# Optimization experiments

Measured on AMD Instinct MI355X. Metric: run time of the kernel, lower is better.

The kernel has to match this reference:

```python
import jax, jax.numpy as jnp
import numpy as np

DIM = 1024
HEADS = 8


def setup_inputs() -> dict:
    key = jax.random.key(0)
    ks = jax.random.split(key, 8)
    b, n, m, nc, d = 2, 1024, 4, 1024, DIM
    x = jax.random.normal(ks[0], (b, n, d), dtype=jnp.float32)
    context = jax.random.normal(ks[1], (b, m, nc, d), dtype=jnp.float32)
    doc_similarities = jax.random.normal(ks[2], (b, m), dtype=jnp.float32)
    # learned params (Linear weights stored as [in, out] for x @ W)
    s = 1.0 / np.sqrt(d)
    Wq = jax.random.uniform(ks[3], (d, d), minval=-s, maxval=s, dtype=jnp.float32)
    Wkv = jax.random.uniform(ks[4], (d, 2 * d), minval=-s, maxval=s, dtype=jnp.float32)
    Wout = jax.random.uniform(ks[5], (d, d), minval=-s, maxval=s, dtype=jnp.float32)
    bout = jax.random.uniform(ks[6], (d,), minval=-s, maxval=s, dtype=jnp.float32)
    beta = jnp.array(1.0, dtype=jnp.float32)
    return {"x": x, "context": context, "doc_similarities": doc_similarities,
            "Wq": Wq, "Wkv": Wkv, "beta": beta, "Wout": Wout, "bout": bout}


def reference(x, context, doc_similarities, Wq, Wkv, beta, Wout, bout):
    b, n, dim = x.shape
    h = HEADS
    hd = dim // h
    scale = dim ** -0.5
    m, nc = context.shape[1], context.shape[2]

    # q: [b, h, n, hd]
    q = (x @ Wq).reshape(b, n, h, hd).transpose(0, 2, 1, 3)

    # flatten docs: [b, m*nc, dim]
    ctx = context.reshape(b, m * nc, dim)
    # doc similarity bias, repeated per token within each doc: [b, m*nc]
    sim = jnp.repeat(doc_similarities, nc, axis=1) * beta

    kv = ctx @ Wkv  # [b, L, 2*dim]
    k, v = jnp.split(kv, 2, axis=-1)
    k = k.reshape(b, m * nc, h, hd).transpose(0, 2, 1, 3)  # [b, h, L, hd]
    v = v.reshape(b, m * nc, h, hd).transpose(0, 2, 1, 3)

    dots = jnp.einsum('bhid,bhjd->bhij', q, k) * scale
    dots = dots + sim[:, None, None, :]
    attn = jax.nn.softmax(dots, axis=-1)
    out = jnp.einsum('bhij,bhjd->bhid', attn, v)
    out = out.transpose(0, 2, 1, 3).reshape(b, n, dim)
    return out @ Wout + bout
```

## Files before the change

### kernel.cpp

```cpp
#include <hip/hip_runtime.h>
#include <stdint.h>

typedef __attribute__((ext_vector_type(4))) float f32x4;
typedef __attribute__((ext_vector_type(8))) __bf16 bf16x8;

__device__ __forceinline__ uint16_t f2bf(float f) {
  uint32_t u = __builtin_bit_cast(uint32_t, f);
  u += 0x7FFFu + ((u >> 16) & 1u);
  return (uint16_t)(u >> 16);
}

__device__ __forceinline__ float bf2f(uint16_t u) {
  uint32_t v = ((uint32_t)u) << 16;
  return __builtin_bit_cast(float, v);
}

__device__ __forceinline__ void load_lds16(const uint16_t* g, uint16_t* l) {
  __builtin_amdgcn_global_load_lds((const __attribute__((address_space(1))) void*)g,
                                   (__attribute__((address_space(3))) void*)l, 16, 0, 0);
}

__global__ __launch_bounds__(256) void k_prep(const float* __restrict__ x,
                                              const float* __restrict__ ctx,
                                              const float* __restrict__ Wq,
                                              const float* __restrict__ Wkv,
                                              const float* __restrict__ Wout,
                                              uint16_t* __restrict__ xb,
                                              uint16_t* __restrict__ ctxb,
                                              uint16_t* __restrict__ wqt,
                                              uint16_t* __restrict__ wkvt,
                                              uint16_t* __restrict__ woutt,
                                              float qscale) {
  __shared__ float tile[32][33];
  int id = blockIdx.x;
  int tid = threadIdx.x;
  if (id < 10240) {
    const float* in;
    uint16_t* out;
    int j = id * 256 + tid;
    if (j < 524288) { in = x; out = xb; }
    else            { in = ctx; out = ctxb; j -= 524288; }
    float4 v = ((const float4*)in)[j];
    union { uint16_t u[4]; uint64_t q; } o;
    o.u[0] = f2bf(v.x); o.u[1] = f2bf(v.y); o.u[2] = f2bf(v.z); o.u[3] = f2bf(v.w);
    ((uint64_t*)out)[j] = o.q;
    return;
  }
  id -= 10240;
  const float* W;
  uint16_t* Wt;
  int N, n0, k0;
  float sc = 1.0f;
  if (id < 1024)      { W = Wq;   Wt = wqt;   N = 1024; sc = qscale;
                        n0 = (id & 31) * 32; k0 = (id >> 5) * 32; }
  else if (id < 2048) { W = Wout; Wt = woutt; N = 1024; id -= 1024;
                        n0 = (id & 31) * 32; k0 = (id >> 5) * 32; }
  else                { W = Wkv;  Wt = wkvt;  N = 2048; id -= 2048;
                        n0 = (id & 63) * 32; k0 = (id >> 6) * 32; }
  int c = tid & 31, r0 = tid >> 5;
#pragma unroll
  for (int i = 0; i < 4; i++) {
    int r = r0 + i * 8;
    tile[r][c] = W[(size_t)(k0 + r) * N + n0 + c];
  }
  __syncthreads();
#pragma unroll
  for (int i = 0; i < 4; i++) {
    int r = r0 + i * 8;
    Wt[(size_t)(n0 + r) * 1024 + k0 + c] = f2bf(tile[c][r] * sc);
  }
}

__global__ __launch_bounds__(256, 4) void k_gemm_fused(const uint16_t* __restrict__ ctxb,
                                                       const uint16_t* __restrict__ wkvt,
                                                       const uint16_t* __restrict__ xb,
                                                       const uint16_t* __restrict__ wqt,
                                                       uint16_t* __restrict__ kb,
                                                       uint16_t* __restrict__ vtb,
                                                       uint16_t* __restrict__ qb) {
  __shared__ uint16_t smem[16384];
  const int K = 1024;
  const int tid = threadIdx.x;
  const int lane = tid & 63, w = tid >> 6;
  const int quad = lane >> 4, l16 = lane & 15;
  const int wr = (w >> 1) * 64, wc = (w & 1) * 64;
  int id = blockIdx.x;
  int bx, by, isQ;
  const uint16_t *Ab, *Bb;
  if (id < 1024) {
    isQ = 0;
    int xcd = id & 7, t = id >> 3;
    by = (xcd << 3) + (t & 7);
    bx = t >> 3;
    Ab = ctxb + (size_t)by * 128 * K;
    Bb = wkvt + (size_t)bx * 128 * K;
  } else {
    isQ = 1; id -= 1024;
    int xcd = id & 7, t = id >> 3;
    by = (xcd << 1) + (t & 1);
    bx = t >> 1;
    Ab = xb + (size_t)by * 128 * K;
    Bb = wqt + (size_t)bx * 128 * K;
  }
  f32x4 acc[4][4] = {};
  const int rA = tid >> 2, slotA = tid & 3;
  const int rA1 = rA + 64;
  const int segA0 = (slotA ^ ((rA + (rA >> 2)) & 3)) * 8;
  const int segA1 = (slotA ^ ((rA1 + (rA1 >> 2)) & 3)) * 8;
  const uint16_t* gA0 = Ab + (size_t)rA * K + segA0;
  const uint16_t* gA1 = Ab + (size_t)rA1 * K + segA1;
  const uint16_t* gB0 = Bb + (size_t)rA * K + segA0;
  const uint16_t* gB1 = Bb + (size_t)rA1 * K + segA1;
  load_lds16(gA0, smem + tid * 8);
  load_lds16(gA1, smem + (tid + 256) * 8);
  load_lds16(gB0, smem + (tid + 512) * 8);
  load_lds16(gB1, smem + (tid + 768) * 8);
  for (int t = 0; t < 32; ++t) {
    const uint16_t* la = smem + (t & 1) * 8192;
    const uint16_t* lb = la + 4096;
    if (t < 31) {
      uint16_t* ln = smem + ((t + 1) & 1) * 8192;
      const int k1 = (t + 1) * 32;
      load_lds16(gA0 + k1, ln + tid * 8);
      load_lds16(gA1 + k1, ln + (tid + 256) * 8);
      load_lds16(gB0 + k1, ln + (tid + 512) * 8);
      load_lds16(gB1 + k1, ln + (tid + 768) * 8);
      asm volatile("s_waitcnt vmcnt(4)\n\ts_barrier" ::: "memory");
    } else {
      asm volatile("s_waitcnt vmcnt(0)\n\ts_barrier" ::: "memory");
    }
    bf16x8 af[4], bfr[4];
#pragma unroll
    for (int i = 0; i < 4; i++) {
      int R = wr + i * 16 + l16;
      int s = quad ^ ((R + (R >> 2)) & 3);
      af[i] = *(const bf16x8*)&la[R * 32 + s * 8];
    }
#pragma unroll
    for (int j = 0; j < 4; j++) {
      int R = wc + j * 16 + l16;
      int s = quad ^ ((R + (R >> 2)) & 3);
      bfr[j] = *(const bf16x8*)&lb[R * 32 + s * 8];
    }
    __builtin_amdgcn_s_setprio(1);
#pragma unroll
    for (int i = 0; i < 4; i++)
#pragma unroll
      for (int j = 0; j < 4; j++)
        acc[i][j] = __builtin_amdgcn_mfma_f32_16x16x32_bf16(af[i], bfr[j], acc[i][j], 0, 0, 0);
    __builtin_amdgcn_s_setprio(0);
    asm volatile("s_barrier" ::: "memory");
  }
  __syncthreads();
  if (isQ) {
#pragma unroll
    for (int i = 0; i < 4; i++)
#pragma unroll
      for (int j = 0; j < 4; j++) {
        size_t row = (size_t)by * 128 + wr + i * 16 + quad * 4;
        size_t col = (size_t)bx * 128 + wc + j * 16 + l16;
#pragma unroll
        for (int r = 0; r < 4; r++)
          qb[(row + r) * 1024 + col] = f2bf(acc[i][j][r]);
      }
  } else if (bx < 8) {
#pragma unroll
    for (int i = 0; i < 4; i++)
#pragma unroll
      for (int j = 0; j < 4; j++) {
        int rowg = by * 128 + wr + i * 16 + quad * 4;
        int bb = rowg >> 12, l = rowg & 4095;
        int c = wc + j * 16 + l16;
        uint16_t* dst = kb + (((size_t)(bb * 8 + bx) * 4096 + l) * 128 + c);
#pragma unroll
        for (int r = 0; r < 4; r++)
          dst[r * 128] = f2bf(acc[i][j][r]);
      }
  } else {
    const int bh = (by >> 5) * 8 + (bx - 8);
    const int lbase = (by & 31) * 128;
    uint16_t* vdst = vtb + (size_t)bh * 524288;
#pragma unroll
    for (int half = 0; half < 2; half++) {
      if (wr == half * 64) {
#pragma unroll
        for (int i = 0; i < 4; i++)
#pragma unroll
          for (int j = 0; j < 4; j++) {
            int rowl = i * 16 + quad * 4;
            int col = wc + j * 16 + l16;
            union { uint64_t q; uint16_t u[4]; } pk;
#pragma unroll
            for (int r = 0; r < 4; r++) pk.u[r] = f2bf(acc[i][j][r]);
            *(uint64_t*)&smem[col * 72 + rowl] = pk.q;
          }
      }
      __syncthreads();
      {
        int col = tid >> 1, rseg = (tid & 1) * 32;
        const uint16_t* src = &smem[col * 72 + rseg];
        uint16_t* d = vdst + (size_t)col * 4096 + lbase + half * 64 + rseg;
#pragma unroll
        for (int k = 0; k < 4; k++)
          ((uint4*)d)[k] = *(const uint4*)&src[k * 8];
      }
      __syncthreads();
    }
  }
}

__global__ __launch_bounds__(256) void k_gemm64(const uint16_t* __restrict__ A,
                                                const uint16_t* __restrict__ Bt,
                                                float* __restrict__ Cf,
                                                const float* __restrict__ bias,
                                                int M, int N, int K) {
  __shared__ uint16_t smem[16384];
  const int tid = threadIdx.x;
  const int lane = tid & 63, w = tid >> 6;
  const int quad = lane >> 4, l16 = lane & 15;
  const int wr = (w >> 1) * 32, wc = (w & 1) * 32;
  const size_t tr0 = (size_t)blockIdx.y * 64, tc0 = (size_t)blockIdx.x * 64;
  f32x4 acc[2][2] = {};
  const int rS = tid >> 3, sS = tid & 7;
  const int seg = (sS ^ (rS & 7)) * 8;
  const uint16_t* Ab = A + tr0 * K;
  const uint16_t* Bb = Bt + tc0 * K;
  const uint16_t* gA0 = Ab + (size_t)rS * K + seg;
  const uint16_t* gA1 = Ab + (size_t)(rS + 32) * K + seg;
  const uint16_t* gB0 = Bb + (size_t)rS * K + seg;
  const uint16_t* gB1 = Bb + (size_t)(rS + 32) * K + seg;
  const int NT = K >> 6;
  load_lds16(gA0, smem + tid * 8);
  load_lds16(gA1, smem + (tid + 256) * 8);
  load_lds16(gB0, smem + (tid + 512) * 8);
  load_lds16(gB1, smem + (tid + 768) * 8);
  for (int t = 0; t < NT; ++t) {
    const uint16_t* la = smem + (t & 1) * 8192;
    const uint16_t* lb = la + 4096;
    if (t < NT - 1) {
      uint16_t* ln = smem + ((t + 1) & 1) * 8192;
      const int k1 = (t + 1) * 64;
      load_lds16(gA0 + k1, ln + tid * 8);
      load_lds16(gA1 + k1, ln + (tid + 256) * 8);
      load_lds16(gB0 + k1, ln + (tid + 512) * 8);
      load_lds16(gB1 + k1, ln + (tid + 768) * 8);
      asm volatile("s_waitcnt vmcnt(4)\n\ts_barrier" ::: "memory");
    } else {
      asm volatile("s_waitcnt vmcnt(0)\n\ts_barrier" ::: "memory");
    }
    __builtin_amdgcn_s_setprio(1);
#pragma unroll
    for (int sub = 0; sub < 2; sub++) {
      const int kk = sub * 4 + quad;
      bf16x8 af[2], bfr[2];
#pragma unroll
      for (int i = 0; i < 2; i++) {
        int R = wr + i * 16 + l16;
        af[i] = *(const bf16x8*)&la[R * 64 + (kk ^ (R & 7)) * 8];
      }
#pragma unroll
      for (int j = 0; j < 2; j++) {
        int R = wc + j * 16 + l16;
        bfr[j] = *(const bf16x8*)&lb[R * 64 + (kk ^ (R & 7)) * 8];
      }
#pragma unroll
      for (int i = 0; i < 2; i++)
#pragma unroll
        for (int j = 0; j < 2; j++)
          acc[i][j] = __builtin_amdgcn_mfma_f32_16x16x32_bf16(af[i], bfr[j], acc[i][j], 0, 0, 0);
    }
    __builtin_amdgcn_s_setprio(0);
    asm volatile("s_barrier" ::: "memory");
  }
#pragma unroll
  for (int i = 0; i < 2; i++) {
#pragma unroll
    for (int j = 0; j < 2; j++) {
      size_t row = tr0 + wr + i * 16 + quad * 4;
      size_t col = tc0 + wc + j * 16 + l16;
#pragma unroll
      for (int r = 0; r < 4; r++)
        Cf[(row + r) * N + col] = acc[i][j][r] + bias[col];
    }
  }
}

__global__ __launch_bounds__(256) void k_attn(const uint16_t* __restrict__ q,
                                              const uint16_t* __restrict__ kb,
                                              const uint16_t* __restrict__ vt,
                                              const float* __restrict__ sims,
                                              const float* __restrict__ beta,
                                              uint16_t* __restrict__ po,
                                              float* __restrict__ pl) {
  __shared__ uint16_t Kl[2][8192];
  __shared__ uint16_t Vl[2][8192];
  __shared__ uint16_t Pl[4096];
  const int idx = blockIdx.x;
  const int qbx = idx >> 7, g = idx & 127;
  const int h = g >> 4, b = (g >> 3) & 1, sp = g & 7;
  const int q0 = qbx * 128;
  const int tid = threadIdx.x, lane = tid & 63, w = tid >> 6;
  const int quad = lane >> 4, l16 = lane & 15;
  const float wsplit =
      __builtin_amdgcn_exp2f(sims[b * 4 + (sp >> 1)] * beta[0] * 1.44269504f);
  uint16_t* Pw = Pl + w * 1024;

  union { uint32_t u[4]; bf16x8 v; } Oc;
#pragma unroll
  for (int j = 0; j < 4; j++) Oc.u[j] = 0x3F803F80u;
  const bf16x8 onesf = Oc.v;

  bf16x8 qf[2][4];
#pragma unroll
  for (int rb = 0; rb < 2; rb++) {
    const uint16_t* qrow =
        q + ((size_t)(b * 1024 + q0 + w * 32 + rb * 16 + l16)) * 1024 + h * 128 + quad * 8;
#pragma unroll
    for (int ks = 0; ks < 4; ks++) qf[rb][ks] = *(const bf16x8*)(qrow + ks * 32);
  }
  f32x4 o[2][8] = {};
  f32x4 o9[2] = {};

  const uint16_t* kptr = kb + ((size_t)(b * 8 + h) * 4096 + sp * 512) * 128;
  const uint16_t* vptr = vt + ((size_t)(b * 8 + h) * 128) * 4096 + sp * 512;

#pragma unroll
  for (int ii = 0; ii < 4; ii++) {
    int g2 = tid + ii * 256;
    int row = g2 >> 4, seg = (g2 & 15) ^ (row & 15);
    load_lds16(kptr + row * 128 + seg * 8, &Kl[0][g2 * 8]);
  }
#pragma unroll
  for (int ii = 0; ii < 4; ii++) {
    int g2 = tid + ii * 256;
    int row = g2 >> 3, seg = (g2 & 7) ^ (row & 7);
    load_lds16(vptr + (size_t)row * 4096 + seg * 8, &Vl[0][g2 * 8]);
  }

  for (int c = 0; c < 8; c++) {
    const uint16_t* Kc = Kl[c & 1];
    const uint16_t* Vc = Vl[c & 1];
    if (c < 7) {
      const uint16_t* kn = kptr + 64 * 128;
      const uint16_t* vn = vptr + 64;
      uint16_t* Kd = Kl[(c + 1) & 1];
      uint16_t* Vd = Vl[(c + 1) & 1];
#pragma unroll
      for (int ii = 0; ii < 4; ii++) {
        int g2 = tid + ii * 256;
        int row = g2 >> 4, seg = (g2 & 15) ^ (row & 15);
        load_lds16(kn + row * 128 + seg * 8, Kd + g2 * 8);
      }
#pragma unroll
      for (int ii = 0; ii < 4; ii++) {
        int g2 = tid + ii * 256;
        int row = g2 >> 3, seg = (g2 & 7) ^ (row & 7);
        load_lds16(vn + (size_t)row * 4096 + seg * 8, Vd + g2 * 8);
      }
      asm volatile("s_waitcnt vmcnt(8)\n\ts_barrier" ::: "memory");
    } else {
      asm volatile("s_waitcnt vmcnt(0)\n\ts_barrier" ::: "memory");
    }
#pragma unroll
    for (int kh = 0; kh < 2; kh++) {
#pragma unroll
      for (int nb2 = 0; nb2 < 2; nb2++) {
        const int nb = kh * 2 + nb2;
        f32x4 s0 = {}, s1 = {};
        __builtin_amdgcn_s_setprio(1);
#pragma unroll
        for (int ks = 0; ks < 4; ks++) {
          bf16x8 kf = *(const bf16x8*)&Kc[(nb * 16 + l16) * 128 + (((ks * 4 + quad) ^ l16) * 8)];
          s0 = __builtin_amdgcn_mfma_f32_16x16x32_bf16(qf[0][ks], kf, s0, 0, 0, 0);
          s1 = __builtin_amdgcn_mfma_f32_16x16x32_bf16(qf[1][ks], kf, s1, 0, 0, 0);
        }
        __builtin_amdgcn_s_setprio(0);
        const int sl = nb2 * 2 + (l16 >> 3);
#pragma unroll
        for (int r = 0; r < 4; r++) {
          int rp0 = quad * 4 + r;
          Pw[rp0 * 32 + ((sl ^ ((rp0 >> 1) & 3)) * 8) + (l16 & 7)] =
              f2bf(__builtin_amdgcn_exp2f(s0[r]));
          int rp1 = 16 + rp0;
          Pw[rp1 * 32 + ((sl ^ ((rp1 >> 1) & 3)) * 8) + (l16 & 7)] =
              f2bf(__builtin_amdgcn_exp2f(s1[r]));
        }
      }
      __asm__ volatile("s_waitcnt lgkmcnt(0)" ::: "memory");
      const int segp = (quad ^ ((l16 >> 1) & 3)) * 8;
      bf16x8 pf0 = *(const bf16x8*)&Pw[l16 * 32 + segp];
      bf16x8 pf1 = *(const bf16x8*)&Pw[(16 + l16) * 32 + segp];
      const int sq = ((kh * 4 + quad) ^ (l16 & 7)) * 8;
      __builtin_amdgcn_s_setprio(1);
#pragma unroll
      for (int nb = 0; nb < 8; nb++) {
        bf16x8 vf = *(const bf16x8*)&Vc[(nb * 16 + l16) * 64 + sq];
        o[0][nb] = __builtin_amdgcn_mfma_f32_16x16x32_bf16(pf0, vf, o[0][nb], 0, 0, 0);
        o[1][nb] = __builtin_amdgcn_mfma_f32_16x16x32_bf16(pf1, vf, o[1][nb], 0, 0, 0);
      }
      o9[0] = __builtin_amdgcn_mfma_f32_16x16x32_bf16(pf0, onesf, o9[0], 0, 0, 0);
      o9[1] = __builtin_amdgcn_mfma_f32_16x16x32_bf16(pf1, onesf, o9[1], 0, 0, 0);
      __builtin_amdgcn_s_setprio(0);
    }
    asm volatile("s_barrier" ::: "memory");
    kptr += 64 * 128;
    vptr += 64;
  }
  const int rowbase = (sp * 16 + b * 8 + h) * 1024 + q0 + w * 32;
#pragma unroll
  for (int rb = 0; rb < 2; rb++)
#pragma unroll
    for (int r = 0; r < 4; r++) {
      int row = rowbase + rb * 16 + quad * 4 + r;
#pragma unroll
      for (int nb = 0; nb < 8; nb++)
        po[(size_t)row * 128 + nb * 16 + l16] = f2bf(o[rb][nb][r] * wsplit);
      if (l16 == 0)
        pl[row] = o9[rb][r] * wsplit;
    }
}

__global__ __launch_bounds__(256) void k_merge(const uint16_t* __restrict__ po,
                                               const float* __restrict__ pl,
                                               uint16_t* __restrict__ attb) {
  const int bq = blockIdx.x;
  const int b = bq >> 10, qi = bq & 1023;
  const int t = threadIdx.x;
  const int h = t >> 5, d0 = (t & 31) * 4;
  const int bh = b * 8 + h;
  float den = 0.f;
  float acc[4] = {0.f, 0.f, 0.f, 0.f};
#pragma unroll
  for (int s = 0; s < 8; s++) {
    den += pl[(s * 16 + bh) * 1024 + qi];
    union { uint64_t q; uint16_t u[4]; } v;
    v.q = *(const uint64_t*)&po[(((size_t)(s * 16 + bh)) * 1024 + qi) * 128 + d0];
#pragma unroll
    for (int j = 0; j < 4; j++) acc[j] += bf2f(v.u[j]);
  }
  const float inv = 1.0f / den;
  union { uint64_t q; uint16_t u[4]; } o;
#pragma unroll
  for (int j = 0; j < 4; j++) o.u[j] = f2bf(acc[j] * inv);
  *(uint64_t*)&attb[((size_t)(b * 1024 + qi)) * 1024 + h * 128 + d0] = o.q;
}

extern "C" void kernel_launch(void* const* d_in, const int* in_sizes, int n_in,
                              void* d_out, int out_size, void* d_ws, size_t ws_size,
                              hipStream_t stream) {
  (void)in_sizes; (void)n_in; (void)out_size; (void)ws_size;
  const float* x    = (const float*)d_in[0];
  const float* ctx  = (const float*)d_in[1];
  const float* sims = (const float*)d_in[2];
  const float* Wq   = (const float*)d_in[3];
  const float* Wkv  = (const float*)d_in[4];
  const float* beta = (const float*)d_in[5];
  const float* Wout = (const float*)d_in[6];
  const float* bout = (const float*)d_in[7];
  float* out = (float*)d_out;

  char* ws = (char*)d_ws;
  uint16_t* xb    = (uint16_t*)(ws + 0);
  uint16_t* ctxb  = (uint16_t*)(ws + (4u << 20));
  uint16_t* wqt   = (uint16_t*)(ws + (20u << 20));
  uint16_t* wkvt  = (uint16_t*)(ws + (22u << 20));
  uint16_t* kb    = (uint16_t*)(ws + (32u << 20));
  uint16_t* vtb   = (uint16_t*)(ws + (48u << 20));
  float*    pl    = (float*)   (ws + (64u << 20));
  uint16_t* woutt = (uint16_t*)(ws + (68u << 20));
  uint16_t* qb    = (uint16_t*)(ws + (70u << 20));
  uint16_t* attb  = (uint16_t*)(ws + (74u << 20));
  uint16_t* po = (uint16_t*)(ws + 0);

  const float LOG2E = 1.44269504f;
  const float qscale = 0.03125f * LOG2E;

  k_prep<<<14336, 256, 0, stream>>>(x, ctx, Wq, Wkv, Wout, xb, ctxb, wqt, wkvt, woutt, qscale);
  k_gemm_fused<<<1152, 256, 0, stream>>>(ctxb, wkvt, xb, wqt, kb, vtb, qb);
  k_attn<<<1024, 256, 0, stream>>>(qb, kb, vtb, sims, beta, po, pl);
  k_merge<<<2048, 256, 0, stream>>>(po, pl, attb);
  k_gemm64<<<dim3(16, 32), 256, 0, stream>>>(attb, woutt, out, bout, 2048, 1024, 1024);
}
```

Before: 221.7 us.

## Keep attention probabilities in registers via transposed QK MFMA and permlane swaps

Computes S^T by swapping the MFMA operands, so each lane holds the probabilities it needs for the PV MFMA A-operand. It then packs them to bf16 with v_cvt_pk_bf16_f32 and rearranges them across lanes with permlane32/16 swaps. This removes the LDS round trip for P: the shared-memory writes, the lgkmcnt wait and the reads, plus the Pl buffer. The risk is getting the lane permutation exactly right, and a fallback to shuffles if the builtins are missing, which would be slower.

```diff
diff --git a/kernel.cpp b/kernel.cpp
--- a/kernel.cpp
+++ b/kernel.cpp
@@ -3,6 +3,7 @@
 
 typedef __attribute__((ext_vector_type(4))) float f32x4;
 typedef __attribute__((ext_vector_type(8))) __bf16 bf16x8;
+typedef __attribute__((ext_vector_type(2))) unsigned int u32x2;
 
 __device__ __forceinline__ uint16_t f2bf(float f) {
   uint32_t u = __builtin_bit_cast(uint32_t, f);
@@ -13,6 +14,40 @@
 __device__ __forceinline__ float bf2f(uint16_t u) {
   uint32_t v = ((uint32_t)u) << 16;
   return __builtin_bit_cast(float, v);
+}
+
+__device__ __forceinline__ uint32_t cvtpk_bf16(float lo, float hi) {
+  uint32_t r;
+  asm("v_cvt_pk_bf16_f32 %0, %1, %2" : "=v"(r) : "v"(lo), "v"(hi));
+  return r;
+}
+
+__device__ __forceinline__ void swap_half32(uint32_t& a, uint32_t& b) {
+#if __has_builtin(__builtin_amdgcn_permlane32_swap)
+  u32x2 r = __builtin_amdgcn_permlane32_swap(a, b, false, false);
+  a = r[0]; b = r[1];
+#else
+  int lane = __builtin_amdgcn_mbcnt_hi(~0u, __builtin_amdgcn_mbcnt_lo(~0u, 0));
+  uint32_t ax = (uint32_t)__shfl_xor((int)a, 32, 64);
+  uint32_t bx = (uint32_t)__shfl_xor((int)b, 32, 64);
+  uint32_t an = (lane < 32) ? a : bx;
+  uint32_t bn = (lane < 32) ? ax : b;
+  a = an; b = bn;
+#endif
+}
+
+__device__ __forceinline__ void swap_half16(uint32_t& a, uint32_t& b) {
+#if __has_builtin(__builtin_amdgcn_permlane16_swap)
+  u32x2 r = __builtin_amdgcn_permlane16_swap(a, b, false, false);
+  a = r[0]; b = r[1];
+#else
+  int lane = __builtin_amdgcn_mbcnt_hi(~0u, __builtin_amdgcn_mbcnt_lo(~0u, 0));
+  uint32_t ax = (uint32_t)__shfl_xor((int)a, 16, 64);
+  uint32_t bx = (uint32_t)__shfl_xor((int)b, 16, 64);
+  uint32_t an = ((lane & 16) == 0) ? a : bx;
+  uint32_t bn = ((lane & 16) == 0) ? ax : b;
+  a = an; b = bn;
+#endif
 }
 
 __device__ __forceinline__ void load_lds16(const uint16_t* g, uint16_t* l) {
@@ -294,7 +329,6 @@
                                               float* __restrict__ pl) {
   __shared__ uint16_t Kl[2][8192];
   __shared__ uint16_t Vl[2][8192];
-  __shared__ uint16_t Pl[4096];
   const int idx = blockIdx.x;
   const int qbx = idx >> 7, g = idx & 127;
   const int h = g >> 4, b = (g >> 3) & 1, sp = g & 7;
@@ -303,7 +337,6 @@
   const int quad = lane >> 4, l16 = lane & 15;
   const float wsplit =
       __builtin_amdgcn_exp2f(sims[b * 4 + (sp >> 1)] * beta[0] * 1.44269504f);
-  uint16_t* Pw = Pl + w * 1024;
 
   union { uint32_t u[4]; bf16x8 v; } Oc;
 #pragma unroll
@@ -363,43 +396,49 @@
     }
 #pragma unroll
     for (int kh = 0; kh < 2; kh++) {
+      f32x4 s[2][2] = {{{0.f,0.f,0.f,0.f},{0.f,0.f,0.f,0.f}},
+                       {{0.f,0.f,0.f,0.f},{0.f,0.f,0.f,0.f}}};
+      __builtin_amdgcn_s_setprio(1);
 #pragma unroll
       for (int nb2 = 0; nb2 < 2; nb2++) {
         const int nb = kh * 2 + nb2;
-        f32x4 s0 = {}, s1 = {};
-        __builtin_amdgcn_s_setprio(1);
 #pragma unroll
         for (int ks = 0; ks < 4; ks++) {
           bf16x8 kf = *(const bf16x8*)&Kc[(nb * 16 + l16) * 128 + (((ks * 4 + quad) ^ l16) * 8)];
-          s0 = __builtin_amdgcn_mfma_f32_16x16x32_bf16(qf[0][ks], kf, s0, 0, 0, 0);
-          s1 = __builtin_amdgcn_mfma_f32_16x16x32_bf16(qf[1][ks], kf, s1, 0, 0, 0);
+          s[nb2][0] = __builtin_amdgcn_mfma_f32_16x16x32_bf16(kf, qf[0][ks], s[nb2][0], 0, 0, 0);
+          s[nb2][1] = __builtin_amdgcn_mfma_f32_16x16x32_bf16(kf, qf[1][ks], s[nb2][1], 0, 0, 0);
         }
-        __builtin_amdgcn_s_setprio(0);
-        const int sl = nb2 * 2 + (l16 >> 3);
-#pragma unroll
-        for (int r = 0; r < 4; r++) {
-          int rp0 = quad * 4 + r;
-          Pw[rp0 * 32 + ((sl ^ ((rp0 >> 1) & 3)) * 8) + (l16 & 7)] =
-              f2bf(__builtin_amdgcn_exp2f(s0[r]));
-          int rp1 = 16 + rp0;
-          Pw[rp1 * 32 + ((sl ^ ((rp1 >> 1) & 3)) * 8) + (l16 & 7)] =
-              f2bf(__builtin_amdgcn_exp2f(s1[r]));
-        }
-      }
-      __asm__ volatile("s_waitcnt lgkmcnt(0)" ::: "memory");
-      const int segp = (quad ^ ((l16 >> 1) & 3)) * 8;
-      bf16x8 pf0 = *(const bf16x8*)&Pw[l16 * 32 + segp];
-      bf16x8 pf1 = *(const bf16x8*)&Pw[(16 + l16) * 32 + segp];
+      }
+      __builtin_amdgcn_s_setprio(0);
+      bf16x8 pa[2];
+#pragma unroll
+      for (int qh = 0; qh < 2; qh++) {
+        uint32_t a0 = cvtpk_bf16(__builtin_amdgcn_exp2f(s[0][qh][0]),
+                                 __builtin_amdgcn_exp2f(s[0][qh][1]));
+        uint32_t a1 = cvtpk_bf16(__builtin_amdgcn_exp2f(s[0][qh][2]),
+                                 __builtin_amdgcn_exp2f(s[0][qh][3]));
+        uint32_t b0 = cvtpk_bf16(__builtin_amdgcn_exp2f(s[1][qh][0]),
+                                 __builtin_amdgcn_exp2f(s[1][qh][1]));
+        uint32_t b1 = cvtpk_bf16(__builtin_amdgcn_exp2f(s[1][qh][2]),
+                                 __builtin_amdgcn_exp2f(s[1][qh][3]));
+        swap_half32(a0, b0);
+        swap_half16(a0, b0);
+        swap_half32(a1, b1);
+        swap_half16(a1, b1);
+        union { uint32_t u[4]; bf16x8 v; } pk_;
+        pk_.u[0] = a0; pk_.u[1] = a1; pk_.u[2] = b0; pk_.u[3] = b1;
+        pa[qh] = pk_.v;
+      }
       const int sq = ((kh * 4 + quad) ^ (l16 & 7)) * 8;
       __builtin_amdgcn_s_setprio(1);
 #pragma unroll
       for (int nb = 0; nb < 8; nb++) {
         bf16x8 vf = *(const bf16x8*)&Vc[(nb * 16 + l16) * 64 + sq];
-        o[0][nb] = __builtin_amdgcn_mfma_f32_16x16x32_bf16(pf0, vf, o[0][nb], 0, 0, 0);
-        o[1][nb] = __builtin_amdgcn_mfma_f32_16x16x32_bf16(pf1, vf, o[1][nb], 0, 0, 0);
-      }
-      o9[0] = __builtin_amdgcn_mfma_f32_16x16x32_bf16(pf0, onesf, o9[0], 0, 0, 0);
-      o9[1] = __builtin_amdgcn_mfma_f32_16x16x32_bf16(pf1, onesf, o9[1], 0, 0, 0);
+        o[0][nb] = __builtin_amdgcn_mfma_f32_16x16x32_bf16(pa[0], vf, o[0][nb], 0, 0, 0);
+        o[1][nb] = __builtin_amdgcn_mfma_f32_16x16x32_bf16(pa[1], vf, o[1][nb], 0, 0, 0);
+      }
+      o9[0] = __builtin_amdgcn_mfma_f32_16x16x32_bf16(pa[0], onesf, o9[0], 0, 0, 0);
+      o9[1] = __builtin_amdgcn_mfma_f32_16x16x32_bf16(pa[1], onesf, o9[1], 0, 0, 0);
       __builtin_amdgcn_s_setprio(0);
     }
     asm volatile("s_barrier" ::: "memory");
```

Result: faster. 216.8 us (-2.2%).
